# Kernel optimization log

Hardware: AMD Instinct MI355X
Metric: run time of the kernel (lower is better)

## Reference

```python
import jax, jax.numpy as jnp
import numpy as np

B, H, W, D, C, K, ITERS = 16, 64, 64, 64, 16, 5, 4
EPS_LN = 1e-5

def _ln(x, g, b):
    m = x.mean(-1, keepdims=True)
    v = jnp.mean((x - m) ** 2, axis=-1, keepdims=True)
    return (x - m) / jnp.sqrt(v + EPS_LN) * g + b

def _build_grid(h, w):
    # (h, w, 2) with x in [-1,1] over width, y in [-1,1] over height
    y, x = jnp.meshgrid(jnp.linspace(-1.0, 1.0, h), jnp.linspace(-1.0, 1.0, w), indexing='ij')
    return jnp.stack([x, y], axis=-1)

def _forward(feat, feat_color, mask, slot_noise, slots_mu, slots_logsigma,
             w_grid, b_grid, w_k, w_v, ln_kv_g, ln_kv_b, w_mlp, b_mlp,
             ln_q_g, ln_q_b, w_q, w_ih, w_hh, b_ih, b_hh,
             ln_feat_g, ln_feat_b, ln_color_g, ln_color_b,
             ln_res_g, ln_res_b, w_res, b_res):
    b, h, w, d = feat.shape
    n = h * w
    k_slots = mask.shape[0]
    scale = d ** (-0.5)

    grid = _build_grid(h, w)  # (H, W, 2)

    # fg position: weighted mean of grid under mask -> (K, 2), broadcast to (B, K, 2)
    gm = grid.transpose(2, 0, 1)[None] * mask            # (K, 2, H, W)
    fg_pos = gm.sum((2, 3)) / (mask.sum((2, 3)) + 1e-5)  # (K, 2)
    fg_pos = jnp.broadcast_to(fg_pos[None], (b, k_slots, 2))

    feat_n = _ln(feat.reshape(b, n, d), ln_feat_g, ln_feat_b)                    # (B, N, D)
    featc_n = _ln(feat_color.reshape(b, n, feat_color.shape[-1]), ln_color_g, ln_color_b)

    slot = slots_mu + jnp.exp(slots_logsigma) * slot_noise  # (B, K, D)

    # k/v with relative positional grid embedding (fg_pos is constant across iters,
    # so k/v are iteration-invariant and computed once -- same math as the original loop)
    rel = grid[None, None] - fg_pos[:, :, None, None, :]        # (B, K, H, W, 2)
    rel4 = jnp.concatenate([rel, -rel], -1).reshape(b, k_slots, n, 4)
    grid_embed = rel4 @ w_grid.T + b_grid                       # (B, K, N, D)
    k = _ln(feat_n @ w_k.T[None] [0][None][0][None][0] if False else (feat_n @ w_k.T)[:, None] + grid_embed, ln_kv_g, ln_kv_b) @ w_mlp.T + b_mlp
    v = _ln((feat_n @ w_v.T)[:, None] + grid_embed, ln_kv_g, ln_kv_b) @ w_mlp.T + b_mlp

    attn = None
    for it in range(ITERS):
        prev = slot
        q = _ln(slot, ln_q_g, ln_q_b) @ w_q.T                         # (B, K, D)
        logits = jnp.einsum('bkd,bknd->bkn', q, k) * scale
        attn = jax.nn.softmax(logits, axis=-1)                        # (B, K, N)
        upd = jnp.einsum('bkn,bknd->bkd', attn, v)                    # (B, K, D)
        if it != ITERS - 1:
            # torch GRUCell
            x = upd.reshape(-1, d)
            hp = slot.reshape(-1, d)
            gi = x @ w_ih.T + b_ih
            gh = hp @ w_hh.T + b_hh
            i_r, i_z, i_n = jnp.split(gi, 3, axis=-1)
            h_r, h_z, h_n = jnp.split(gh, 3, axis=-1)
            r = jax.nn.sigmoid(i_r + h_r)
            z = jax.nn.sigmoid(i_z + h_z)
            nn_ = jnp.tanh(i_n + r * h_n)
            slot = ((1.0 - z) * nn_ + z * hp).reshape(b, k_slots, d)
            slot = _ln(slot, ln_res_g, ln_res_b) @ w_res.T + b_res + prev
        else:
            slot_color = jnp.einsum('bkn,bnc->bkc', attn, featc_n)
            slot = jnp.concatenate([slot, slot_color], axis=-1)       # (B, K, D+C)

    amin = attn.min(axis=2, keepdims=True)
    amax = attn.max(axis=2, keepdims=True)
    attn = (attn - amin) / (amax - amin + 1e-5)
    return slot, fg_pos, attn

def setup_inputs() -> dict:
    key = jax.random.key(0)
    ks = jax.random.split(key, 16)
    def rn(i, shape, s=0.02):
        return jax.random.normal(ks[i], shape, jnp.float32) * s
    return {
        'feat': jax.random.normal(ks[0], (B, H, W, D), jnp.float32),
        'feat_color': jax.random.normal(ks[1], (B, H, W, C), jnp.float32),
        'mask': jax.random.uniform(ks[2], (K, 1, H, W), jnp.float32),
        'slot_noise': jax.random.normal(ks[3], (B, K, D), jnp.float32),
        'slots_mu': rn(4, (1, 1, D), 1.0),
        'slots_logsigma': rn(5, (1, 1, D), 0.01),
        'w_grid': rn(6, (D, 4)), 'b_grid': jnp.zeros((D,), jnp.float32),
        'w_k': rn(7, (D, D)), 'w_v': rn(8, (D, D)),
        'ln_kv_g': jnp.ones((D,), jnp.float32), 'ln_kv_b': jnp.zeros((D,), jnp.float32),
        'w_mlp': rn(9, (D, D)), 'b_mlp': jnp.zeros((D,), jnp.float32),
        'ln_q_g': jnp.ones((D,), jnp.float32), 'ln_q_b': jnp.zeros((D,), jnp.float32),
        'w_q': rn(10, (D, D)),
        'w_ih': rn(11, (3 * D, D)), 'w_hh': rn(12, (3 * D, D)),
        'b_ih': jnp.zeros((3 * D,), jnp.float32), 'b_hh': jnp.zeros((3 * D,), jnp.float32),
        'ln_feat_g': jnp.ones((D,), jnp.float32), 'ln_feat_b': jnp.zeros((D,), jnp.float32),
        'ln_color_g': jnp.ones((C,), jnp.float32), 'ln_color_b': jnp.zeros((C,), jnp.float32),
        'ln_res_g': jnp.ones((D,), jnp.float32), 'ln_res_b': jnp.zeros((D,), jnp.float32),
        'w_res': rn(13, (D, D)), 'b_res': jnp.zeros((D,), jnp.float32),
    }

def reference(feat, feat_color, mask, slot_noise, slots_mu, slots_logsigma,
              w_grid, b_grid, w_k, w_v, ln_kv_g, ln_kv_b, w_mlp, b_mlp,
              ln_q_g, ln_q_b, w_q, w_ih, w_hh, b_ih, b_hh,
              ln_feat_g, ln_feat_b, ln_color_g, ln_color_b,
              ln_res_g, ln_res_b, w_res, b_res):
    return _forward(feat, feat_color, mask, slot_noise, slots_mu, slots_logsigma,
                    w_grid, b_grid, w_k, w_v, ln_kv_g, ln_kv_b, w_mlp, b_mlp,
                    ln_q_g, ln_q_b, w_q, w_ih, w_hh, b_ih, b_hh,
                    ln_feat_g, ln_feat_b, ln_color_g, ln_color_b,
                    ln_res_g, ln_res_b, w_res, b_res)
```

## Files before the change

### kernel.cpp

```cpp
#include <hip/hip_runtime.h>
#include <stdint.h>

#define B_ 16
#define H_ 64
#define W_ 64
#define D_ 64
#define C_ 16
#define K_ 5
#define N_ 4096
#define NC_ 32
#define CS_ 128
#define EPS 1e-5f

typedef __attribute__((ext_vector_type(8))) short bf16x8;
typedef __attribute__((ext_vector_type(4))) float f32x4;

__device__ __forceinline__ float wsum64(float v){
  #pragma unroll
  for(int o=1;o<64;o<<=1) v += __shfl_xor(v,o,64);
  return v;
}
__device__ __forceinline__ float wmax64(float v){
  #pragma unroll
  for(int o=1;o<64;o<<=1) v = fmaxf(v, __shfl_xor(v,o,64));
  return v;
}
__device__ __forceinline__ float wmin64(float v){
  #pragma unroll
  for(int o=1;o<64;o<<=1) v = fminf(v, __shfl_xor(v,o,64));
  return v;
}
__device__ __forceinline__ uint16_t f2bf(float f){
  uint32_t u = __float_as_uint(f);
  u += 0x7fffu + ((u>>16)&1u);
  return (uint16_t)(u>>16);
}

__global__ __launch_bounds__(256) void k_pre(
    const float* __restrict__ mask, const float* __restrict__ noise,
    const float* __restrict__ mu, const float* __restrict__ lsg,
    const float* __restrict__ wm, const float* __restrict__ bm, const float* __restrict__ lnkb,
    const float* __restrict__ wk, const float* __restrict__ wv, const float* __restrict__ lnfb,
    const float* __restrict__ wq, const float* __restrict__ lnqg, const float* __restrict__ lnqb,
    const float* __restrict__ wres, const float* __restrict__ bres,
    const float* __restrict__ lnrg, const float* __restrict__ lnrb,
    const float* __restrict__ wih, const float* __restrict__ whh,
    const float* __restrict__ wg, const float* __restrict__ bg,
    float* __restrict__ ws_fg, float* __restrict__ out_fg,
    float* __restrict__ bm2, float* __restrict__ fkb, float* __restrict__ fvb,
    float* __restrict__ qb, float* __restrict__ br2,
    float* __restrict__ wgx, float* __restrict__ wgy, float* __restrict__ gscal,
    float* __restrict__ wqpT, float* __restrict__ wrpT,
    float* __restrict__ wvT, float* __restrict__ wmT,
    float* __restrict__ gw, float* __restrict__ slot, float* __restrict__ out_slot){
  int bid=blockIdx.x, tid=threadIdx.x;
  if(bid<5){
    int k=bid;
    float sm=0.f, sx=0.f, sy=0.f;
    for(int p=tid; p<H_*W_; p+=256){
      int i=p>>6, j=p&63;
      float m = mask[k*H_*W_ + p];
      float x = -1.f + (2.f/63.f)*j;
      float y = -1.f + (2.f/63.f)*i;
      sm+=m; sx+=m*x; sy+=m*y;
    }
    __shared__ float r0[4], r1[4], r2[4];
    int wid=tid>>6, lane=tid&63;
    sm=wsum64(sm); sx=wsum64(sx); sy=wsum64(sy);
    if(lane==0){ r0[wid]=sm; r1[wid]=sx; r2[wid]=sy; }
    __syncthreads();
    if(tid==0){
      float tm=r0[0]+r0[1]+r0[2]+r0[3];
      float tx=r1[0]+r1[1]+r1[2]+r1[3];
      float ty=r2[0]+r2[1]+r2[2]+r2[3];
      float px = tx/(tm+1e-5f), py = ty/(tm+1e-5f);
      ws_fg[k*2+0]=px; ws_fg[k*2+1]=py;
      for(int b=0;b<B_;b++){ out_fg[(b*K_+k)*2+0]=px; out_fg[(b*K_+k)*2+1]=py; }
    }
  } else if(bid==5){
    int sel=tid>>6, o=tid&63; float s=0.f;
    if(sel==0){ s=bm[o]; for(int d=0;d<64;d++) s+=lnkb[d]*wm[o*64+d]; bm2[o]=s; }
    else if(sel==1){ for(int d=0;d<64;d++) s+=lnqb[d]*wq[o*64+d]; qb[o]=0.125f*s; }
    else if(sel==2){ for(int d=0;d<64;d++) s+=lnrb[d]*wres[o*64+d]; br2[o]=s+bres[o]; }
    else { for(int d=0;d<64;d++) s+=lnfb[d]*wk[o*64+d]; fkb[o]=s; }
  } else if(bid==6){
    int wv4=tid>>6, l=tid&63;
    if(wv4==0){ float s=0.f; for(int d=0;d<64;d++) s+=lnfb[d]*wv[l*64+d]; fvb[l]=s; }
    else if(wv4==1){
      float4 w4 = *(const float4*)(wg + l*4);
      wgx[l]=w4.x-w4.z; wgy[l]=w4.y-w4.w;
    } else if(wv4==2){
      float4 w4 = *(const float4*)(wg + l*4);
      float wx=w4.x-w4.z, wy=w4.y-w4.w, bl=bg[l];
      float t;
      t=wsum64(wx);    if(l==0) gscal[0]=t*(1.f/64.f);
      t=wsum64(wy);    if(l==0) gscal[1]=t*(1.f/64.f);
      t=wsum64(bl);    if(l==0) gscal[2]=t*(1.f/64.f);
      t=wsum64(wx*wx); if(l==0) gscal[3]=t*(1.f/64.f);
      t=wsum64(wy*wy); if(l==0) gscal[4]=t*(1.f/64.f);
      t=wsum64(wx*wy); if(l==0) gscal[5]=t*(2.f/64.f);
      t=wsum64(wx*bl); if(l==0) gscal[6]=t*(2.f/64.f);
      t=wsum64(wy*bl); if(l==0) gscal[7]=t*(2.f/64.f);
      t=wsum64(bl*bl); if(l==0) gscal[8]=t*(1.f/64.f);
    } else {
      for(int j=l;j<B_*K_*16;j+=64){ int bk2=j>>4, cc2=j&15; out_slot[bk2*80+64+cc2]=0.f; }
    }
  } else if(bid<71){
    int i=(bid-7)*256+tid;
    int a=i>>12, r=i&4095, d=r>>6, o=r&63;
    if(a==0)      wqpT[r]=0.125f*lnqg[d]*wq[o*64+d];
    else if(a==1) wrpT[r]=lnrg[d]*wres[o*64+d];
    else if(a==2) wvT[r]=wv[o*64+d];
    else          wmT[r]=wm[o*64+d];
  } else if(bid<167){
    int i=(bid-71)*256+tid;
    int g6=i>>12, r=i&4095, d=r>>6, o=r&63;
    float v = (g6<3)? wih[(g6*64+o)*64+d] : whh[((g6-3)*64+o)*64+d];
    gw[g6*4096 + d*64 + o] = v;
  } else {
    int i=(bid-167)*256+tid;
    if(i<B_*K_*D_){ int d=i&63; slot[i]=mu[d]+expf(lsg[d])*noise[i]; }
  }
}

__global__ __launch_bounds__(256) void k_featln(const float* __restrict__ feat,
    const float* __restrict__ wk, const float* __restrict__ wv, const float* __restrict__ gf,
    const float* __restrict__ fkb, const float* __restrict__ fvb,
    const float* __restrict__ wgx, const float* __restrict__ wgy, const float* __restrict__ bg,
    const float* __restrict__ fc, const float* __restrict__ gc, const float* __restrict__ bc,
    uint16_t* __restrict__ Aout, float4* __restrict__ kstat, float4* __restrict__ vstat,
    float* __restrict__ fcn){
  int tid=threadIdx.x, wid=tid>>6, lane=tid&63;
  int q=lane>>4, c=lane&15;
  size_t row = (size_t)blockIdx.x*64 + wid*16 + c;
  const float* xp = feat + row*64;
  float x[16];
  *(float4*)&x[0]  = *(const float4*)(xp + q*8);
  *(float4*)&x[4]  = *(const float4*)(xp + q*8 + 4);
  *(float4*)&x[8]  = *(const float4*)(xp + 32 + q*8);
  *(float4*)&x[12] = *(const float4*)(xp + 36 + q*8);
  float s=0.f;
  #pragma unroll
  for(int i=0;i<16;i++) s+=x[i];
  s += __shfl_xor(s,16,64); s += __shfl_xor(s,32,64);
  float mean = s*(1.f/64.f);
  float v=0.f;
  #pragma unroll
  for(int i=0;i<16;i++){ float d=x[i]-mean; v+=d*d; }
  v += __shfl_xor(v,16,64); v += __shfl_xor(v,32,64);
  float rs = rsqrtf(v*(1.f/64.f)+EPS);
  float gl[16];
  *(float4*)&gl[0]  = *(const float4*)(gf + q*8);
  *(float4*)&gl[4]  = *(const float4*)(gf + q*8 + 4);
  *(float4*)&gl[8]  = *(const float4*)(gf + 32 + q*8);
  *(float4*)&gl[12] = *(const float4*)(gf + 36 + q*8);
  bf16x8 A0, A1;
  #pragma unroll
  for(int j=0;j<8;j++){
    A0[j] = (short)f2bf((x[j]  -mean)*rs);
    A1[j] = (short)f2bf((x[8+j]-mean)*rs);
  }
  *(bf16x8*)(Aout + row*64 + q*8) = A0;
  *(bf16x8*)(Aout + row*64 + 32 + q*8) = A1;
  float wgxl[4][4], wgyl[4][4], bgl[4][4];
  #pragma unroll
  for(int ot=0;ot<4;ot++){
    *(float4*)&wgxl[ot][0] = *(const float4*)(wgx + ot*16 + q*4);
    *(float4*)&wgyl[ot][0] = *(const float4*)(wgy + ot*16 + q*4);
    *(float4*)&bgl[ot][0]  = *(const float4*)(bg + ot*16 + q*4);
  }
  #pragma unroll
  for(int mat=0;mat<2;mat++){
    const float* w = mat? wv : wk;
    const float* fb = mat? fvb : fkb;
    float ss=0.f, s2=0.f, dx=0.f, dy=0.f, db=0.f;
    #pragma unroll
    for(int ot=0; ot<4; ot++){
      const float* wp = w + (size_t)(ot*16+c)*64 + q*8;
      bf16x8 W0, W1;
      #pragma unroll
      for(int j=0;j<8;j++){ W0[j]=(short)f2bf(wp[j]*gl[j]); W1[j]=(short)f2bf(wp[32+j]*gl[8+j]); }
      float4 bq = *(const float4*)(fb + ot*16 + q*4);
      f32x4 acc = {bq.x,bq.y,bq.z,bq.w};
      acc = __builtin_amdgcn_mfma_f32_16x16x32_bf16(W0, A0, acc, 0,0,0);
      acc = __builtin_amdgcn_mfma_f32_16x16x32_bf16(W1, A1, acc, 0,0,0);
      #pragma unroll
      for(int r=0;r<4;r++){
        float a=acc[r];
        ss+=a; s2+=a*a;
        dx = fmaf(a, wgxl[ot][r], dx);
        dy = fmaf(a, wgyl[ot][r], dy);
        db = fmaf(a, bgl[ot][r], db);
      }
    }
    ss += __shfl_xor(ss,16,64); ss += __shfl_xor(ss,32,64);
    s2 += __shfl_xor(s2,16,64); s2 += __shfl_xor(s2,32,64);
    dx += __shfl_xor(dx,16,64); dx += __shfl_xor(dx,32,64);
    dy += __shfl_xor(dy,16,64); dy += __shfl_xor(dy,32,64);
    db += __shfl_xor(db,16,64); db += __shfl_xor(db,32,64);
    if(lane<16){
      size_t row2 = (size_t)blockIdx.x*64 + wid*16 + lane;
      float4 st = { ss*(1.f/64.f), s2*(1.f/64.f)+db*(1.f/32.f), dx*(1.f/32.f), dy*(1.f/32.f) };
      (mat? vstat : kstat)[row2] = st;
    }
  }
  int r16=tid>>4, cc=tid&15;
  #pragma unroll
  for(int i=0;i<4;i++){
    size_t row2 = (size_t)blockIdx.x*64 + i*16 + r16;
    float xv = fc[row2*16+cc];
    float sc=xv;
    #pragma unroll
    for(int o=1;o<16;o<<=1) sc += __shfl_xor(sc,o,16);
    float m2 = sc*(1.f/16.f);
    float df = xv-m2;
    float v2 = df*df;
    #pragma unroll
    for(int o=1;o<16;o<<=1) v2 += __shfl_xor(v2,o,16);
    fcn[row2*16+cc] = df*rsqrtf(v2*(1.f/16.f)+EPS)*gc[cc] + bc[cc];
  }
}

template<bool GRU>
__global__ __launch_bounds__(256) void k_slotq(
    const float* __restrict__ slot_prev, float* __restrict__ slot_cur,
    const float* __restrict__ part, const float* __restrict__ pscal,
    const float* __restrict__ red_in,
    const float* __restrict__ gw,
    const float* __restrict__ bih, const float* __restrict__ bhh,
    const float* __restrict__ wrpT, const float* __restrict__ br2,
    const float* __restrict__ wqpT, const float* __restrict__ qb,
    const float* __restrict__ wm, const float* __restrict__ wk,
    const float* __restrict__ lnfg, const float* __restrict__ lnkg,
    const float* __restrict__ fkb, const float* __restrict__ bm2, const float* __restrict__ fvb,
    const float* __restrict__ wvT, const float* __restrict__ wmT,
    const float* __restrict__ wgx, const float* __restrict__ wgy, const float* __restrict__ bg,
    const float* __restrict__ gscal,
    float* __restrict__ qs_out, float* __restrict__ cst_out){
  __shared__ float vv[64], vh[64];
  __shared__ float red6[4][64][6];
  __shared__ float lamb[NC_];
  int bk=blockIdx.x;
  int tid=threadIdx.x, wid=tid>>6, lane=tid&63;
  int o=lane, qq=wid;
  float mwgx=gscal[0], mwgy=gscal[1], mbg=gscal[2];

  #define MV(Wptr) { float p_=0.f; \
      _Pragma("unroll") \
      for(int dd=0;dd<16;dd++) p_ = fmaf(vv[qq*16+dd], (Wptr)[(qq*16+dd)*64+o], p_); \
      red6[qq][o][0]=p_; } __syncthreads();
  #define SUM0 (red6[0][lane][0]+red6[1][lane][0]+red6[2][lane][0]+red6[3][lane][0])

  float cur=0.f, qv=0.f, qp=0.f, hp=0.f;
  if(GRU){
    float As=0.f, Ax=0.f, Ay=0.f, Am=0.f;
    if(wid==0){
      float m_l = (lane<NC_)? red_in[((size_t)bk*NC_+lane)*4]   : -1e30f;
      float s_l = (lane<NC_)? red_in[((size_t)bk*NC_+lane)*4+1] : 0.f;
      float M = wmax64(m_l);
      float eu = (lane<NC_)? __expf(m_l-M) : 0.f;
      float S = wsum64(s_l*eu);
      float lam = eu/S;
      if(lane<NC_) lamb[lane]=lam;
      float p0 = (lane<NC_)? pscal[((size_t)bk*NC_+lane)*4+0] : 0.f;
      float p1 = (lane<NC_)? pscal[((size_t)bk*NC_+lane)*4+1] : 0.f;
      float p2 = (lane<NC_)? pscal[((size_t)bk*NC_+lane)*4+2] : 0.f;
      float p3 = (lane<NC_)? pscal[((size_t)bk*NC_+lane)*4+3] : 0.f;
      As = wsum64(lam*p0); Ax = wsum64(lam*p1);
      Ay = wsum64(lam*p2); Am = wsum64(lam*p3);
    }
    __syncthreads();
    {
      float p_=0.f;
      #pragma unroll
      for(int j=0;j<8;j++){
        int cc = qq*8+j;
        p_ = fmaf(lamb[cc], part[((size_t)bk*NC_+cc)*64+o], p_);
      }
      red6[qq][o][0]=p_;
    }
    __syncthreads();
    if(wid==0){
      float sA = SUM0;
      vv[lane] = lnfg[lane]*sA;
    }
    __syncthreads();
    MV(wvT);
    if(wid==0){
      float fvs = SUM0 + fvb[lane]*As;
      float zs = fvs + Ax*wgx[lane] + Ay*wgy[lane] + As*bg[lane] - Am;
      vv[lane] = lnkg[lane]*zs;
    }
    __syncthreads();
    MV(wmT);
    if(wid==0){
      float x_ = SUM0 + bm2[lane];
      hp = slot_prev[bk*64+lane];
      vv[lane]=x_; vh[lane]=hp;
    }
    __syncthreads();
    {
      float p0=0.f,p1=0.f,p2=0.f,p3=0.f,p4=0.f,p5=0.f;
      #pragma unroll
      for(int dd=0;dd<16;dd++){
        int d = qq*16+dd;
        float xd=vv[d], hd=vh[d];
        p0 = fmaf(xd, gw[d*64+o], p0);
        p1 = fmaf(xd, gw[4096+d*64+o], p1);
        p2 = fmaf(xd, gw[8192+d*64+o], p2);
        p3 = fmaf(hd, gw[12288+d*64+o], p3);
        p4 = fmaf(hd, gw[16384+d*64+o], p4);
        p5 = fmaf(hd, gw[20480+d*64+o], p5);
      }
      red6[qq][o][0]=p0; red6[qq][o][1]=p1; red6[qq][o][2]=p2;
      red6[qq][o][3]=p3; red6[qq][o][4]=p4; red6[qq][o][5]=p5;
    }
    __syncthreads();
    if(wid==0){
      float gir=bih[lane], giz=bih[64+lane], gin=bih[128+lane];
      float ghr=bhh[lane], ghz=bhh[64+lane], ghn=bhh[128+lane];
      #pragma unroll
      for(int w=0;w<4;w++){
        gir+=red6[w][lane][0]; giz+=red6[w][lane][1]; gin+=red6[w][lane][2];
        ghr+=red6[w][lane][3]; ghz+=red6[w][lane][4]; ghn+=red6[w][lane][5];
      }
      float r=1.f/(1.f+__expf(-(gir+ghr)));
      float z=1.f/(1.f+__expf(-(giz+ghz)));
      float nn=tanhf(gin+r*ghn);
      float sp=(1.f-z)*nn+z*hp;
      float m=wsum64(sp)*(1.f/64.f); float df=sp-m;
      float var=wsum64(df*df)*(1.f/64.f);
      vv[lane]=df*rsqrtf(var+EPS);
    }
    __syncthreads();
    MV(wrpT);
    if(wid==0){
      cur = SUM0 + br2[lane] + hp;
      slot_cur[bk*64+lane]=cur;
    }
  } else {
    if(wid==0) cur = slot_prev[bk*64+lane];
  }
  __syncthreads();
  if(wid==0){
    float m=wsum64(cur)*(1.f/64.f); float df=cur-m;
    float var=wsum64(df*df)*(1.f/64.f);
    vv[lane]=df*rsqrtf(var+EPS);
  }
  __syncthreads();
  MV(wqpT);
  if(wid==0){ qv = SUM0 + qb[lane]; vv[lane]=qv; }
  __syncthreads();
  MV(wm);
  if(wid==0){ qp = SUM0*lnkg[lane]; vv[lane]=qp; }
  __syncthreads();
  MV(wk);
  if(wid==0){
    qs_out[bk*64+lane] = SUM0*lnfg[lane];
    float s1 = wsum64(qp);
    float c1 = wsum64(qp*wgx[lane]);
    float c2 = wsum64(qp*wgy[lane]);
    float c3 = wsum64(qp*(bg[lane]+fkb[lane]));
    float c4c = wsum64(qv*bm2[lane]);
    if(lane==0){
      float* cp = cst_out + bk*8;
      cp[0]=c1-s1*mwgx; cp[1]=c2-s1*mwgy; cp[2]=c3-s1*mbg; cp[3]=s1; cp[4]=c4c;
    }
  }
  #undef MV
  #undef SUM0
}

template<bool FINAL>
__global__ __launch_bounds__(256) void k_attn(const uint16_t* __restrict__ Aw,
    const float4* __restrict__ kstat, const float4* __restrict__ vstat,
    const float* __restrict__ qsg, const float* __restrict__ cstg,
    const float* __restrict__ gscal, const float* __restrict__ ws_fg,
    float* __restrict__ lgt, float* __restrict__ red_out,
    float* __restrict__ part_o, float* __restrict__ pscal_o){
  __shared__ uint32_t As_[CS_*32];
  __shared__ float dps[5][CS_+4];
  __shared__ float pw[4][5][64];
  __shared__ float rm[2][5], rn[2][5];
  __shared__ float rsc[2][5][5];
  __shared__ float cstl[5][5];
  __shared__ float fgl[5][2];
  int chunk=blockIdx.x, b=blockIdx.y;
  int tid=threadIdx.x, wid=tid>>6, lane=tid&63;
  int c=lane&15, q=lane>>4;
  float mwgx=gscal[0], mwgy=gscal[1], mbg=gscal[2];
  float g1=gscal[3], g2=gscal[4], g3=gscal[5], g4=gscal[6], g5=gscal[7], g6=gscal[8];

  const uint4* Ag = (const uint4*)(Aw + ((size_t)b*N_ + chunk*CS_)*64);
  #pragma unroll
  for(int jj=0;jj<4;jj++){
    int f = jj*256 + tid;
    *(uint4*)(As_ + f*4) = Ag[f];
  }
  if(tid<25) cstl[tid/5][tid%5] = cstg[(b*K_ + tid/5)*8 + (tid%5)];
  if(tid>=32 && tid<42){ int i2=tid-32; fgl[i2>>1][i2&1] = ws_fg[i2]; }
  bool act = tid < CS_;
  int nrow = chunk*CS_ + (tid & (CS_-1));
  float4 st, sv;
  float gx=0.f, gy=0.f;
  if(act){
    st = kstat[(size_t)b*N_ + nrow];
    if(!FINAL) sv = vstat[(size_t)b*N_ + nrow];
    gx = -1.f + (2.f/63.f)*(nrow&63);
    gy = -1.f + (2.f/63.f)*(nrow>>6);
  }
  __syncthreads();

  {
    bf16x8 QF0={0,0,0,0,0,0,0,0}, QF1={0,0,0,0,0,0,0,0};
    if(c<5){
      const float* qpp = qsg + (b*K_+c)*64;
      #pragma unroll
      for(int j=0;j<8;j++){
        QF0[j] = (short)f2bf(qpp[q*8+j]);
        QF1[j] = (short)f2bf(qpp[32+q*8+j]);
      }
    }
    const uint16_t* Abase = Aw + ((size_t)b*N_ + chunk*CS_)*64;
    #pragma unroll
    for(int it=0;it<2;it++){
      int tile = wid*32 + it*16;
      const uint16_t* rp = Abase + (size_t)(tile+c)*64;
      bf16x8 BF0 = *(const bf16x8*)(rp + q*8);
      bf16x8 BF1 = *(const bf16x8*)(rp + 32 + q*8);
      f32x4 acc = {0.f,0.f,0.f,0.f};
      acc = __builtin_amdgcn_mfma_f32_16x16x32_bf16(QF0, BF0, acc, 0,0,0);
      acc = __builtin_amdgcn_mfma_f32_16x16x32_bf16(QF1, BF1, acc, 0,0,0);
      #pragma unroll
      for(int r=0;r<4;r++){
        int s = q*4+r;
        if(s<5) dps[s][tile+c]=acc[r];
      }
    }
  }
  __syncthreads();

  float l5[5], w5[5];
  if(act){
    #pragma unroll
    for(int k=0;k<5;k++){
      float rx = gx - fgl[k][0], ry = gy - fgl[k][1];
      float CX=cstl[k][0], CY=cstl[k][1], C0=cstl[k][2], S1=cstl[k][3], C4=cstl[k][4];
      float quad = g1*rx*rx + g2*ry*ry + g3*rx*ry + g4*rx + g5*ry + g6;
      float mu = st.x + rx*mwgx + ry*mwgy + mbg;
      float var = st.y + rx*st.z + ry*st.w + quad - mu*mu;
      float rsn = rsqrtf(var+EPS);
      float l = rsn*(dps[k][tid] + rx*CX + ry*CY + C0 - S1*st.x) + C4;
      l5[k]=l;
      float wmx = wmax64(l);
      if(lane==0) rm[wid][k]=wmx;
      if(FINAL){ float mn=wmin64(l); if(lane==0) rn[wid][k]=mn; }
    }
  }
  __syncthreads();
  if(act){
    #pragma unroll
    for(int k=0;k<5;k++){
      float m_c = fmaxf(rm[0][k], rm[1][k]);
      float e = __expf(l5[k]-m_c);
      float scq = wsum64(e);
      if(!FINAL){
        float rx = gx - fgl[k][0], ry = gy - fgl[k][1];
        float quad = g1*rx*rx + g2*ry*ry + g3*rx*ry + g4*rx + g5*ry + g6;
        float muV = sv.x + rx*mwgx + ry*mwgy + mbg;
        float varV = sv.y + rx*sv.z + ry*sv.w + quad - muV*muV;
        float rsv_ = rsqrtf(varV+EPS);
        float w_ = e*rsv_;
        w5[k]=w_;
        float As2=wsum64(w_), Ax2=wsum64(w_*rx), Ay2=wsum64(w_*ry), Am2=wsum64(w_*muV);
        if(lane==0){ rsc[wid][k][0]=scq; rsc[wid][k][1]=As2; rsc[wid][k][2]=Ax2;
                     rsc[wid][k][3]=Ay2; rsc[wid][k][4]=Am2; }
      } else {
        lgt[(size_t)(b*K_+k)*N_ + nrow] = l5[k];
        if(lane==0) rsc[wid][k][0]=scq;
      }
    }
  }
  __syncthreads();
  if(tid<5){
    int k=tid;
    size_t idx = ((size_t)(b*K_+k)*NC_+chunk)*4;
    red_out[idx+0]=fmaxf(rm[0][k],rm[1][k]);
    red_out[idx+1]=rsc[0][k][0]+rsc[1][k][0];
    if(FINAL) red_out[idx+2]=fminf(rn[0][k],rn[1][k]);
    if(!FINAL){
      pscal_o[idx+0]=rsc[0][k][1]+rsc[1][k][1];
      pscal_o[idx+1]=rsc[0][k][2]+rsc[1][k][2];
      pscal_o[idx+2]=rsc[0][k][3]+rsc[1][k][3];
      pscal_o[idx+3]=rsc[0][k][4]+rsc[1][k][4];
    }
  }
  if(act && !FINAL){
    #pragma unroll
    for(int k=0;k<5;k++) dps[k][tid]=w5[k];
  }

  if(!FINAL){
    __syncthreads();
    const uint16_t* Au = (const uint16_t*)As_;
    float a[5]={0.f,0.f,0.f,0.f,0.f};
    for(int r32=0;r32<32;r32++){
      int row = wid*32 + r32;
      float av = __uint_as_float(((uint32_t)Au[row*64+lane])<<16);
      #pragma unroll
      for(int k=0;k<5;k++) a[k]=fmaf(dps[k][row], av, a[k]);
    }
    #pragma unroll
    for(int k=0;k<5;k++) pw[wid][k][lane]=a[k];
    __syncthreads();
    if(tid<64){
      #pragma unroll
      for(int k=0;k<5;k++){
        float s2 = pw[0][k][tid]+pw[1][k][tid]+pw[2][k][tid]+pw[3][k][tid];
        part_o[((size_t)(b*K_+k)*NC_+chunk)*64 + tid] = s2;
      }
    }
  }
}

__global__ __launch_bounds__(256) void k_fin(const float* __restrict__ lgt,
    const float* __restrict__ red, const float* __restrict__ featc,
    const float* __restrict__ sl1, float* __restrict__ out_slot,
    float* __restrict__ out_attn){
  __shared__ float psp[CS_];
  __shared__ float pcz[4][16];
  int chunk=blockIdx.x, bk=blockIdx.y, b=bk/K_;
  int tid=threadIdx.x, wid=tid>>6, lane=tid&63, sub=lane>>4, c4=lane&15;
  const float* rp = red + (size_t)bk*NC_*4;
  float M=-1e30f;
  #pragma unroll
  for(int i=0;i<NC_;i++) M = fmaxf(M, rp[i*4]);
  float S=0.f;
  #pragma unroll
  for(int i=0;i<NC_;i++) S += rp[i*4+1]*__expf(rp[i*4]-M);
  float invS = 1.f/S;
  float LMIN=1e30f;
  #pragma unroll
  for(int i=0;i<NC_;i++) LMIN=fminf(LMIN, rp[i*4+2]);
  float amin = __expf(LMIN-M)*invS;
  float dinv = 1.f/(invS - amin + 1e-5f);
  const float* lp = lgt + (size_t)bk*N_ + chunk*CS_;
  if(tid<CS_){
    float p = __expf(lp[tid]-M)*invS;
    psp[tid]=p;
    out_attn[(size_t)bk*N_ + chunk*CS_ + tid] = (p - amin)*dinv;
  }
  __syncthreads();
  const float* Fb = featc + ((size_t)b*N_ + chunk*CS_)*16;
  float ac=0.f;
  for(int t=0;t<8;t++){
    int n = wid*32 + t*4 + sub;
    ac += psp[n]*Fb[(size_t)n*16 + c4];
  }
  ac+=__shfl_xor(ac,16,64); ac+=__shfl_xor(ac,32,64);
  if(lane<16) pcz[wid][lane]=ac;
  __syncthreads();
  if(tid<16){
    float s2 = pcz[0][tid]+pcz[1][tid]+pcz[2][tid]+pcz[3][tid];
    atomicAdd(&out_slot[bk*80+64+tid], s2);
  }
  if(chunk==0 && tid<64) out_slot[bk*80+tid]=sl1[bk*64+tid];
}

extern "C" void kernel_launch(void* const* d_in, const int* in_sizes, int n_in,
                              void* d_out, int out_size, void* d_ws, size_t ws_size,
                              hipStream_t stream){
  (void)in_sizes; (void)n_in; (void)out_size; (void)ws_size;
  const float* feat = (const float*)d_in[0];
  const float* featc= (const float*)d_in[1];
  const float* mask = (const float*)d_in[2];
  const float* noise= (const float*)d_in[3];
  const float* mu   = (const float*)d_in[4];
  const float* lsg  = (const float*)d_in[5];
  const float* wg   = (const float*)d_in[6];
  const float* bg   = (const float*)d_in[7];
  const float* wk   = (const float*)d_in[8];
  const float* wv   = (const float*)d_in[9];
  const float* lnkg = (const float*)d_in[10];
  const float* lnkb = (const float*)d_in[11];
  const float* wm   = (const float*)d_in[12];
  const float* bm   = (const float*)d_in[13];
  const float* lnqg = (const float*)d_in[14];
  const float* lnqb = (const float*)d_in[15];
  const float* wq   = (const float*)d_in[16];
  const float* wih  = (const float*)d_in[17];
  const float* whh  = (const float*)d_in[18];
  const float* bih  = (const float*)d_in[19];
  const float* bhh  = (const float*)d_in[20];
  const float* lnfg = (const float*)d_in[21];
  const float* lnfb = (const float*)d_in[22];
  const float* lncg = (const float*)d_in[23];
  const float* lncb = (const float*)d_in[24];
  const float* lnrg = (const float*)d_in[25];
  const float* lnrb = (const float*)d_in[26];
  const float* wres = (const float*)d_in[27];
  const float* bres = (const float*)d_in[28];

  float* out = (float*)d_out;
  float* out_slot = out;
  float* out_fg   = out + 6400;
  float* out_attn = out + 6560;

  float* wsf     = (float*)d_ws;
  float* ws_fg   = wsf;
  float* ws_bm2  = wsf + 16;
  float* ws_fkb  = ws_bm2 + 64;
  float* ws_fvb  = ws_fkb + 64;
  float* ws_qb   = ws_fvb + 64;
  float* ws_br2  = ws_qb + 64;
  float* ws_wgx  = ws_br2 + 64;
  float* ws_wgy  = ws_wgx + 64;
  float* ws_gs   = ws_wgy + 64;
  float* ws_wqpT = ws_gs + 16;
  float* ws_wrpT = ws_wqpT + 4096;
  float* ws_wvT  = ws_wrpT + 4096;
  float* ws_wmT  = ws_wvT + 4096;
  float* ws_gw   = ws_wmT + 4096;
  float* ws_fc   = ws_gw + 24576;
  float* ws_sl0  = ws_fc + (size_t)B_*N_*C_;
  float* ws_sl1  = ws_sl0 + B_*K_*D_;
  float* ws_qs   = ws_sl1 + B_*K_*D_;
  float* ws_cst  = ws_qs + B_*K_*D_;
  float* ws_lgt  = ws_cst + 640;
  float* ws_red0 = ws_lgt + (size_t)B_*K_*N_;
  float* ws_red1 = ws_red0 + B_*K_*NC_*4;
  float* ws_prt0 = ws_red1 + B_*K_*NC_*4;
  float* ws_prt1 = ws_prt0 + (size_t)B_*K_*NC_*64;
  float* ws_psc0 = ws_prt1 + (size_t)B_*K_*NC_*64;
  float* ws_psc1 = ws_psc0 + B_*K_*NC_*4;
  float4* ws_kst = (float4*)(ws_psc1 + B_*K_*NC_*4);
  float4* ws_vst = ws_kst + (size_t)B_*N_;
  uint16_t* ws_A = (uint16_t*)(ws_vst + (size_t)B_*N_);

  k_pre<<<187,256,0,stream>>>(mask,noise,mu,lsg, wm,bm,lnkb, wk,wv,lnfb,
                              wq,lnqg,lnqb, wres,bres,lnrg,lnrb, wih,whh, wg,bg,
                              ws_fg,out_fg, ws_bm2,ws_fkb,ws_fvb,ws_qb,ws_br2,
                              ws_wgx,ws_wgy,ws_gs,
                              ws_wqpT,ws_wrpT,ws_wvT,ws_wmT, ws_gw, ws_sl0, out_slot);
  k_featln<<<(B_*N_)/64,256,0,stream>>>(feat,wk,wv,lnfg,ws_fkb,ws_fvb,
                                        ws_wgx,ws_wgy,bg,
                                        featc,lncg,lncb,
                                        ws_A,ws_kst,ws_vst,ws_fc);

  dim3 agrid(NC_,B_);
  #define SQ_ARGS(SPREV,SCUR,PIN,SCIN,RIN) SPREV,SCUR,PIN,SCIN,RIN,ws_gw, \
      bih,bhh,ws_wrpT,ws_br2,ws_wqpT,ws_qb, wm,wk,lnfg,lnkg, \
      ws_fkb,ws_bm2,ws_fvb, ws_wvT,ws_wmT, ws_wgx,ws_wgy,bg, ws_gs, ws_qs,ws_cst
  #define AT_ARGS(ROUT,POUT,SCOUT) ws_A,ws_kst,ws_vst,ws_qs,ws_cst,ws_gs,ws_fg, \
      ws_lgt,ROUT,POUT,SCOUT

  k_slotq<false><<<B_*K_,256,0,stream>>>(SQ_ARGS(ws_sl0,ws_sl0,ws_prt1,ws_psc1,ws_red1));
  k_attn<false><<<agrid,256,0,stream>>>(AT_ARGS(ws_red0,ws_prt0,ws_psc0));
  k_slotq<true><<<B_*K_,256,0,stream>>>(SQ_ARGS(ws_sl0,ws_sl1,ws_prt0,ws_psc0,ws_red0));
  k_attn<false><<<agrid,256,0,stream>>>(AT_ARGS(ws_red1,ws_prt1,ws_psc1));
  k_slotq<true><<<B_*K_,256,0,stream>>>(SQ_ARGS(ws_sl1,ws_sl0,ws_prt1,ws_psc1,ws_red1));
  k_attn<false><<<agrid,256,0,stream>>>(AT_ARGS(ws_red0,ws_prt0,ws_psc0));
  k_slotq<true><<<B_*K_,256,0,stream>>>(SQ_ARGS(ws_sl0,ws_sl1,ws_prt0,ws_psc0,ws_red0));
  k_attn<true><<<agrid,256,0,stream>>>(AT_ARGS(ws_red1,ws_prt1,ws_psc1));
  k_fin<<<dim3(NC_,B_*K_),256,0,stream>>>(ws_lgt,ws_red1,ws_fc,ws_sl1,out_slot,out_attn);
}
```

Baseline: 222.6 us.

## Fold chained slot-update matvecs into precomputed composite weight matrices

Precomputes composite matrices (Wq·Wm·Wk with LN gains, and Wv·Wm) plus bias and scalar vectors in two extra k_pre blocks. This collapses the chains of three sequential 64x64 matvecs in k_slotq into one matvec each, cutting the serial sync-bound work per iteration. It also skips the unused A-tile load in the final attention pass and unrolls the weighted-sum loop with float4 LDS reads. The cost is two single-block prep tasks running 64^3 triple loops, which lengthen k_pre, plus slightly different float rounding from reassociation.

```diff
diff --git a/kernel.cpp b/kernel.cpp
--- a/kernel.cpp
+++ b/kernel.cpp
@@ -46,13 +46,19 @@
     const float* __restrict__ lnrg, const float* __restrict__ lnrb,
     const float* __restrict__ wih, const float* __restrict__ whh,
     const float* __restrict__ wg, const float* __restrict__ bg,
+    const float* __restrict__ lnfg, const float* __restrict__ lnkg,
     float* __restrict__ ws_fg, float* __restrict__ out_fg,
     float* __restrict__ bm2, float* __restrict__ fkb, float* __restrict__ fvb,
     float* __restrict__ qb, float* __restrict__ br2,
     float* __restrict__ wgx, float* __restrict__ wgy, float* __restrict__ gscal,
-    float* __restrict__ wqpT, float* __restrict__ wrpT,
-    float* __restrict__ wvT, float* __restrict__ wmT,
-    float* __restrict__ gw, float* __restrict__ slot, float* __restrict__ out_slot){
+    float* __restrict__ wrpT,
+    float* __restrict__ gw, float* __restrict__ slot, float* __restrict__ out_slot,
+    float* __restrict__ WQp, float* __restrict__ WCp, float* __restrict__ bq2p,
+    float* __restrict__ uvp, float* __restrict__ vqp, float* __restrict__ cscp){
+  __shared__ float M0[64][65];
+  __shared__ float M1[64][65];
+  __shared__ float M2[64][65];
+  __shared__ float vtmp[4][64];
   int bid=blockIdx.x, tid=threadIdx.x;
   if(bid<5){
     int k=bid;
@@ -105,21 +111,69 @@
     } else {
       for(int j=l;j<B_*K_*16;j+=64){ int bk2=j>>4, cc2=j&15; out_slot[bk2*80+64+cc2]=0.f; }
     }
-  } else if(bid<71){
+  } else if(bid<23){
     int i=(bid-7)*256+tid;
-    int a=i>>12, r=i&4095, d=r>>6, o=r&63;
-    if(a==0)      wqpT[r]=0.125f*lnqg[d]*wq[o*64+d];
-    else if(a==1) wrpT[r]=lnrg[d]*wres[o*64+d];
-    else if(a==2) wvT[r]=wv[o*64+d];
-    else          wmT[r]=wm[o*64+d];
-  } else if(bid<167){
-    int i=(bid-71)*256+tid;
+    int d=i>>6, o=i&63;
+    wrpT[i]=lnrg[d]*wres[o*64+d];
+  } else if(bid<119){
+    int i=(bid-23)*256+tid;
     int g6=i>>12, r=i&4095, d=r>>6, o=r&63;
     float v = (g6<3)? wih[(g6*64+o)*64+d] : whh[((g6-3)*64+o)*64+d];
     gw[g6*4096 + d*64 + o] = v;
+  } else if(bid<139){
+    int i=(bid-119)*256+tid;
+    if(i<B_*K_*D_){ int d=i&63; slot[i]=mu[d]+expf(lsg[d])*noise[i]; }
+  } else if(bid==139){
+    for(int i=tid;i<4096;i+=256){ int r=i>>6,c2=i&63; M0[r][c2]=wq[i]; M1[r][c2]=wm[i]; }
+    __syncthreads();
+    if(tid<64){ float s=0.f; for(int d=0;d<64;d++) s+=lnqb[d]*M0[tid][d]; vtmp[0][tid]=0.125f*s; }
+    else if(tid<128){ int c2=tid-64; float s=bm[c2]; for(int d=0;d<64;d++) s+=lnkb[d]*M1[c2][d]; vtmp[1][c2]=s; }
+    else if(tid<192){ int o=tid-128; float s=0.f; for(int d=0;d<64;d++) s+=lnfb[d]*wk[o*64+d]; vtmp[2][o]=s; }
+    __syncthreads();
+    for(int i=tid;i<4096;i+=256){ int d=i>>6,e=i&63; float s=0.f;
+      for(int c2=0;c2<64;c2++) s=fmaf(M0[c2][d], M1[c2][e], s);
+      M2[d][e]=0.125f*lnqg[d]*s; }
+    __syncthreads();
+    if(tid<64){
+      int e=tid; float s=0.f; for(int c2=0;c2<64;c2++) s=fmaf(vtmp[0][c2], M1[c2][e], s); vtmp[3][e]=s;
+    } else if(tid<128){
+      int d=tid-64; float s=0.f; for(int c2=0;c2<64;c2++) s=fmaf(M0[c2][d], vtmp[1][c2], s);
+      vqp[4*64+d]=0.125f*lnqg[d]*s;
+    }
+    __syncthreads();
+    for(int i=tid;i<4096;i+=256){ int e=i>>6,o=i&63; M0[e][o]=lnkg[e]*wk[i]; }
+    __syncthreads();
+    for(int i=tid;i<4096;i+=256){ int d=i>>6,o=i&63; float s=0.f;
+      for(int e=0;e<64;e++) s=fmaf(M2[d][e], M0[e][o], s);
+      WQp[i]=lnfg[o]*s; }
+    if(tid<64){ int o=tid; float s=0.f;
+      for(int e=0;e<64;e++) s=fmaf(vtmp[3][e], M0[e][o], s);
+      bq2p[o]=lnfg[o]*s; }
+    else if(tid<128){ int d=tid-64; float s1=0.f,sx=0.f,sy=0.f,s3=0.f;
+      for(int e=0;e<64;e++){ float pe=M2[d][e]*lnkg[e];
+        float gx_=wg[e*4]-wg[e*4+2], gy_=wg[e*4+1]-wg[e*4+3];
+        s1+=pe; sx+=pe*gx_; sy+=pe*gy_; s3+=pe*(bg[e]+vtmp[2][e]); }
+      vqp[0*64+d]=s1; vqp[1*64+d]=sx; vqp[2*64+d]=sy; vqp[3*64+d]=s3; }
+    else if(tid==128){ float c0=0.f,c1=0.f,c2=0.f,c3=0.f,c4=0.f;
+      for(int e=0;e<64;e++){ float qe=vtmp[3][e]*lnkg[e];
+        float gx_=wg[e*4]-wg[e*4+2], gy_=wg[e*4+1]-wg[e*4+3];
+        c0+=qe; c1+=qe*gx_; c2+=qe*gy_; c3+=qe*(bg[e]+vtmp[2][e]);
+        c4+=vtmp[0][e]*vtmp[1][e]; }
+      cscp[0]=c0; cscp[1]=c1; cscp[2]=c2; cscp[3]=c3; cscp[4]=c4; }
   } else {
-    int i=(bid-167)*256+tid;
-    if(i<B_*K_*D_){ int d=i&63; slot[i]=mu[d]+expf(lsg[d])*noise[i]; }
+    for(int i=tid;i<4096;i+=256){ int r=i>>6,c2=i&63; M0[r][c2]=wv[i]*lnkg[r]; M1[r][c2]=wm[i]; }
+    __syncthreads();
+    if(tid<64){ float s=0.f; const float* wr=wv+tid*64;
+      for(int d=0;d<64;d++) s+=lnfb[d]*wr[d]; vtmp[0][tid]=s; }
+    __syncthreads();
+    for(int i=tid;i<4096;i+=256){ int d=i>>6,o=i&63; float s=0.f;
+      for(int e=0;e<64;e++) s=fmaf(M0[e][d], M1[o][e], s);
+      WCp[i]=lnfg[d]*s; }
+    if(tid<64){ int o=tid; float s1=0.f,s2=0.f,s3=0.f,s4=0.f;
+      for(int e=0;e<64;e++){ float we=lnkg[e]*M1[o][e];
+        float gx_=wg[e*4]-wg[e*4+2], gy_=wg[e*4+1]-wg[e*4+3];
+        s1+=we*(vtmp[0][e]+bg[e]); s2+=we*gx_; s3+=we*gy_; s4+=we; }
+      uvp[0*64+o]=s1; uvp[1*64+o]=s2; uvp[2*64+o]=s3; uvp[3*64+o]=s4; }
   }
 }
 
@@ -229,17 +283,16 @@
     const float* __restrict__ gw,
     const float* __restrict__ bih, const float* __restrict__ bhh,
     const float* __restrict__ wrpT, const float* __restrict__ br2,
-    const float* __restrict__ wqpT, const float* __restrict__ qb,
-    const float* __restrict__ wm, const float* __restrict__ wk,
-    const float* __restrict__ lnfg, const float* __restrict__ lnkg,
-    const float* __restrict__ fkb, const float* __restrict__ bm2, const float* __restrict__ fvb,
-    const float* __restrict__ wvT, const float* __restrict__ wmT,
-    const float* __restrict__ wgx, const float* __restrict__ wgy, const float* __restrict__ bg,
+    const float* __restrict__ bm2,
+    const float* __restrict__ WQ, const float* __restrict__ bq2,
+    const float* __restrict__ WC, const float* __restrict__ uvec,
+    const float* __restrict__ vq, const float* __restrict__ csc,
     const float* __restrict__ gscal,
     float* __restrict__ qs_out, float* __restrict__ cst_out){
   __shared__ float vv[64], vh[64];
   __shared__ float red6[4][64][6];
   __shared__ float lamb[NC_];
+  __shared__ float sc4[4];
   int bk=blockIdx.x;
   int tid=threadIdx.x, wid=tid>>6, lane=tid&63;
   int o=lane, qq=wid;
@@ -251,9 +304,8 @@
       red6[qq][o][0]=p_; } __syncthreads();
   #define SUM0 (red6[0][lane][0]+red6[1][lane][0]+red6[2][lane][0]+red6[3][lane][0])
 
-  float cur=0.f, qv=0.f, qp=0.f, hp=0.f;
+  float cur=0.f, hp=0.f;
   if(GRU){
-    float As=0.f, Ax=0.f, Ay=0.f, Am=0.f;
     if(wid==0){
       float m_l = (lane<NC_)? red_in[((size_t)bk*NC_+lane)*4]   : -1e30f;
       float s_l = (lane<NC_)? red_in[((size_t)bk*NC_+lane)*4+1] : 0.f;
@@ -266,8 +318,9 @@
       float p1 = (lane<NC_)? pscal[((size_t)bk*NC_+lane)*4+1] : 0.f;
       float p2 = (lane<NC_)? pscal[((size_t)bk*NC_+lane)*4+2] : 0.f;
       float p3 = (lane<NC_)? pscal[((size_t)bk*NC_+lane)*4+3] : 0.f;
-      As = wsum64(lam*p0); Ax = wsum64(lam*p1);
-      Ay = wsum64(lam*p2); Am = wsum64(lam*p3);
+      float As = wsum64(lam*p0), Ax = wsum64(lam*p1);
+      float Ay = wsum64(lam*p2), Am = wsum64(lam*p3);
+      if(lane==0){ sc4[0]=As; sc4[1]=Ax; sc4[2]=Ay; sc4[3]=Am; }
     }
     __syncthreads();
     {
@@ -280,21 +333,13 @@
       red6[qq][o][0]=p_;
     }
     __syncthreads();
+    if(wid==0) vv[lane] = SUM0;
+    __syncthreads();
+    MV(WC);
     if(wid==0){
-      float sA = SUM0;
-      vv[lane] = lnfg[lane]*sA;
-    }
-    __syncthreads();
-    MV(wvT);
-    if(wid==0){
-      float fvs = SUM0 + fvb[lane]*As;
-      float zs = fvs + Ax*wgx[lane] + Ay*wgy[lane] + As*bg[lane] - Am;
-      vv[lane] = lnkg[lane]*zs;
-    }
-    __syncthreads();
-    MV(wmT);
-    if(wid==0){
-      float x_ = SUM0 + bm2[lane];
+      float As=sc4[0],Ax=sc4[1],Ay=sc4[2],Am=sc4[3];
+      float x_ = SUM0 + As*uvec[lane] + Ax*uvec[64+lane] + Ay*uvec[128+lane]
+               - Am*uvec[192+lane] + bm2[lane];
       hp = slot_prev[bk*64+lane];
       vv[lane]=x_; vh[lane]=hp;
     }
@@ -345,28 +390,21 @@
   if(wid==0){
     float m=wsum64(cur)*(1.f/64.f); float df=cur-m;
     float var=wsum64(df*df)*(1.f/64.f);
-    vv[lane]=df*rsqrtf(var+EPS);
-  }
-  __syncthreads();
-  MV(wqpT);
-  if(wid==0){ qv = SUM0 + qb[lane]; vv[lane]=qv; }
-  __syncthreads();
-  MV(wm);
-  if(wid==0){ qp = SUM0*lnkg[lane]; vv[lane]=qp; }
-  __syncthreads();
-  MV(wk);
-  if(wid==0){
-    qs_out[bk*64+lane] = SUM0*lnfg[lane];
-    float s1 = wsum64(qp);
-    float c1 = wsum64(qp*wgx[lane]);
-    float c2 = wsum64(qp*wgy[lane]);
-    float c3 = wsum64(qp*(bg[lane]+fkb[lane]));
-    float c4c = wsum64(qv*bm2[lane]);
+    float LNc=df*rsqrtf(var+EPS);
+    vv[lane]=LNc;
+    float s1=wsum64(LNc*vq[lane])     + csc[0];
+    float c1=wsum64(LNc*vq[64+lane])  + csc[1];
+    float c2=wsum64(LNc*vq[128+lane]) + csc[2];
+    float c3=wsum64(LNc*vq[192+lane]) + csc[3];
+    float c4=wsum64(LNc*vq[256+lane]) + csc[4];
     if(lane==0){
       float* cp = cst_out + bk*8;
-      cp[0]=c1-s1*mwgx; cp[1]=c2-s1*mwgy; cp[2]=c3-s1*mbg; cp[3]=s1; cp[4]=c4c;
-    }
-  }
+      cp[0]=c1-s1*mwgx; cp[1]=c2-s1*mwgy; cp[2]=c3-s1*mbg; cp[3]=s1; cp[4]=c4;
+    }
+  }
+  __syncthreads();
+  MV(WQ);
+  if(wid==0) qs_out[bk*64+lane] = SUM0 + bq2[lane];
   #undef MV
   #undef SUM0
 }
@@ -379,7 +417,7 @@
     float* __restrict__ lgt, float* __restrict__ red_out,
     float* __restrict__ part_o, float* __restrict__ pscal_o){
   __shared__ uint32_t As_[CS_*32];
-  __shared__ float dps[5][CS_+4];
+  __shared__ __align__(16) float dps[5][CS_+4];
   __shared__ float pw[4][5][64];
   __shared__ float rm[2][5], rn[2][5];
   __shared__ float rsc[2][5][5];
@@ -391,11 +429,13 @@
   float mwgx=gscal[0], mwgy=gscal[1], mbg=gscal[2];
   float g1=gscal[3], g2=gscal[4], g3=gscal[5], g4=gscal[6], g5=gscal[7], g6=gscal[8];
 
-  const uint4* Ag = (const uint4*)(Aw + ((size_t)b*N_ + chunk*CS_)*64);
-  #pragma unroll
-  for(int jj=0;jj<4;jj++){
-    int f = jj*256 + tid;
-    *(uint4*)(As_ + f*4) = Ag[f];
+  if(!FINAL){
+    const uint4* Ag = (const uint4*)(Aw + ((size_t)b*N_ + chunk*CS_)*64);
+    #pragma unroll
+    for(int jj=0;jj<4;jj++){
+      int f = jj*256 + tid;
+      *(uint4*)(As_ + f*4) = Ag[f];
+    }
   }
   if(tid<25) cstl[tid/5][tid%5] = cstg[(b*K_ + tid/5)*8 + (tid%5)];
   if(tid>=32 && tid<42){ int i2=tid-32; fgl[i2>>1][i2&1] = ws_fg[i2]; }
@@ -503,15 +543,27 @@
   if(!FINAL){
     __syncthreads();
     const uint16_t* Au = (const uint16_t*)As_;
-    float a[5]={0.f,0.f,0.f,0.f,0.f};
-    for(int r32=0;r32<32;r32++){
-      int row = wid*32 + r32;
-      float av = __uint_as_float(((uint32_t)Au[row*64+lane])<<16);
-      #pragma unroll
-      for(int k=0;k<5;k++) a[k]=fmaf(dps[k][row], av, a[k]);
-    }
-    #pragma unroll
-    for(int k=0;k<5;k++) pw[wid][k][lane]=a[k];
+    float a0=0.f,a1=0.f,a2=0.f,a3=0.f,a4=0.f;
+    #pragma unroll
+    for(int rb=0;rb<8;rb++){
+      int row0 = wid*32 + rb*4;
+      float4 d0 = *(const float4*)&dps[0][row0];
+      float4 d1 = *(const float4*)&dps[1][row0];
+      float4 d2 = *(const float4*)&dps[2][row0];
+      float4 d3 = *(const float4*)&dps[3][row0];
+      float4 d4 = *(const float4*)&dps[4][row0];
+      float av0 = __uint_as_float(((uint32_t)Au[(row0+0)*64+lane])<<16);
+      float av1 = __uint_as_float(((uint32_t)Au[(row0+1)*64+lane])<<16);
+      float av2 = __uint_as_float(((uint32_t)Au[(row0+2)*64+lane])<<16);
+      float av3 = __uint_as_float(((uint32_t)Au[(row0+3)*64+lane])<<16);
+      a0=fmaf(d0.x,av0,a0); a0=fmaf(d0.y,av1,a0); a0=fmaf(d0.z,av2,a0); a0=fmaf(d0.w,av3,a0);
+      a1=fmaf(d1.x,av0,a1); a1=fmaf(d1.y,av1,a1); a1=fmaf(d1.z,av2,a1); a1=fmaf(d1.w,av3,a1);
+      a2=fmaf(d2.x,av0,a2); a2=fmaf(d2.y,av1,a2); a2=fmaf(d2.z,av2,a2); a2=fmaf(d2.w,av3,a2);
+      a3=fmaf(d3.x,av0,a3); a3=fmaf(d3.y,av1,a3); a3=fmaf(d3.z,av2,a3); a3=fmaf(d3.w,av3,a3);
+      a4=fmaf(d4.x,av0,a4); a4=fmaf(d4.y,av1,a4); a4=fmaf(d4.z,av2,a4); a4=fmaf(d4.w,av3,a4);
+    }
+    pw[wid][0][lane]=a0; pw[wid][1][lane]=a1; pw[wid][2][lane]=a2;
+    pw[wid][3][lane]=a3; pw[wid][4][lane]=a4;
     __syncthreads();
     if(tid<64){
       #pragma unroll
@@ -616,17 +668,20 @@
   float* ws_wgx  = ws_br2 + 64;
   float* ws_wgy  = ws_wgx + 64;
   float* ws_gs   = ws_wgy + 64;
-  float* ws_wqpT = ws_gs + 16;
-  float* ws_wrpT = ws_wqpT + 4096;
-  float* ws_wvT  = ws_wrpT + 4096;
-  float* ws_wmT  = ws_wvT + 4096;
-  float* ws_gw   = ws_wmT + 4096;
-  float* ws_fc   = ws_gw + 24576;
+  float* ws_wrpT = ws_gs + 16;
+  float* ws_gw   = ws_wrpT + 4096;
+  float* ws_WQ   = ws_gw + 24576;
+  float* ws_WC   = ws_WQ + 4096;
+  float* ws_bq2  = ws_WC + 4096;
+  float* ws_u    = ws_bq2 + 64;
+  float* ws_vq   = ws_u + 256;
+  float* ws_csc  = ws_vq + 320;
+  float* ws_qs   = ws_csc + 16;
+  float* ws_cst  = ws_qs + B_*K_*D_;
+  float* ws_fc   = ws_cst + 640;
   float* ws_sl0  = ws_fc + (size_t)B_*N_*C_;
   float* ws_sl1  = ws_sl0 + B_*K_*D_;
-  float* ws_qs   = ws_sl1 + B_*K_*D_;
-  float* ws_cst  = ws_qs + B_*K_*D_;
-  float* ws_lgt  = ws_cst + 640;
+  float* ws_lgt  = ws_sl1 + B_*K_*D_;
   float* ws_red0 = ws_lgt + (size_t)B_*K_*N_;
   float* ws_red1 = ws_red0 + B_*K_*NC_*4;
   float* ws_prt0 = ws_red1 + B_*K_*NC_*4;
@@ -637,11 +692,13 @@
   float4* ws_vst = ws_kst + (size_t)B_*N_;
   uint16_t* ws_A = (uint16_t*)(ws_vst + (size_t)B_*N_);
 
-  k_pre<<<187,256,0,stream>>>(mask,noise,mu,lsg, wm,bm,lnkb, wk,wv,lnfb,
+  k_pre<<<141,256,0,stream>>>(mask,noise,mu,lsg, wm,bm,lnkb, wk,wv,lnfb,
                               wq,lnqg,lnqb, wres,bres,lnrg,lnrb, wih,whh, wg,bg,
+                              lnfg,lnkg,
                               ws_fg,out_fg, ws_bm2,ws_fkb,ws_fvb,ws_qb,ws_br2,
                               ws_wgx,ws_wgy,ws_gs,
-                              ws_wqpT,ws_wrpT,ws_wvT,ws_wmT, ws_gw, ws_sl0, out_slot);
+                              ws_wrpT, ws_gw, ws_sl0, out_slot,
+                              ws_WQ, ws_WC, ws_bq2, ws_u, ws_vq, ws_csc);
   k_featln<<<(B_*N_)/64,256,0,stream>>>(feat,wk,wv,lnfg,ws_fkb,ws_fvb,
                                         ws_wgx,ws_wgy,bg,
                                         featc,lncg,lncb,
@@ -649,8 +706,8 @@
 
   dim3 agrid(NC_,B_);
   #define SQ_ARGS(SPREV,SCUR,PIN,SCIN,RIN) SPREV,SCUR,PIN,SCIN,RIN,ws_gw, \
-      bih,bhh,ws_wrpT,ws_br2,ws_wqpT,ws_qb, wm,wk,lnfg,lnkg, \
-      ws_fkb,ws_bm2,ws_fvb, ws_wvT,ws_wmT, ws_wgx,ws_wgy,bg, ws_gs, ws_qs,ws_cst
+      bih,bhh,ws_wrpT,ws_br2,ws_bm2, ws_WQ,ws_bq2, ws_WC,ws_u, ws_vq,ws_csc, \
+      ws_gs, ws_qs,ws_cst
   #define AT_ARGS(ROUT,POUT,SCOUT) ws_A,ws_kst,ws_vst,ws_qs,ws_cst,ws_gs,ws_fg, \
       ws_lgt,ROUT,POUT,SCOUT
 
```

New measurement: 249.9 us. 1.12x slower.
